# Kernel tuning notes

Hardware: AMD Instinct MI355X
Metric: run time of the kernel (lower is better)

The kernel has to match this reference:

```python
import jax, jax.numpy as jnp
import numpy as np

# Episode config: 4 episodes, 5-way 5-shot, 15 queries/class, 84x84 RGB
B, NTR, NTE, K = 4, 25, 75, 5
H = W = 84
CH = (64, 64, 128, 512)   # 4-block conv backbone channels
NUM_CLASSES = 64
SCALE_CLS = 1.0
EPS = 1e-12


def _l2norm(x, axis):
    # matches torch F.normalize(p=2, eps=1e-12)
    n = jnp.sqrt(jnp.sum(x * x, axis=axis, keepdims=True))
    return x / jnp.maximum(n, EPS)


def _conv_block(x, w, b):
    y = jax.lax.conv_general_dilated(x, w, (1, 1), 'SAME',
                                     dimension_numbers=('NCHW', 'OIHW', 'NCHW'))
    y = jax.nn.relu(y + b[None, :, None, None])
    return jax.lax.reduce_window(y, -jnp.inf, jax.lax.max,
                                 (1, 1, 2, 2), (1, 1, 2, 2), 'VALID')


def _backbone(x, ws, bs):
    for w, b in zip(ws, bs):
        x = _conv_block(x, w, b)
    return x  # (N, 512, 5, 5)


def setup_inputs() -> dict:
    key = jax.random.key(0)
    ks = jax.random.split(key, 16)
    xtrain = jax.random.normal(ks[0], (B, NTR, 3, H, W), jnp.float32)
    xtest = jax.random.normal(ks[1], (B, NTE, 3, H, W), jnp.float32)
    # one-hot support labels: 5 examples per class
    labels_tr = jnp.tile(jnp.arange(K), NTR // K)  # (NTR,)
    ytrain = jnp.tile(jax.nn.one_hot(labels_tr, K, dtype=jnp.float32)[None], (B, 1, 1))
    ytest = jax.random.randint(ks[2], (B, NTE), 0, K)
    # backbone conv params (He init)
    params = {}
    cin = 3
    for i, cout in enumerate(CH):
        scale = np.sqrt(2.0 / (cin * 9)).astype(np.float32)
        params[f'w{i+1}'] = jax.random.normal(ks[3 + i], (cout, cin, 3, 3), jnp.float32) * scale
        params[f'b{i+1}'] = jnp.zeros((cout,), jnp.float32)
        cin = cout
    params['wc'] = jax.random.normal(ks[10], (NUM_CLASSES, CH[-1]), jnp.float32) * np.sqrt(1.0 / CH[-1]).astype(np.float32)
    params['bc'] = jnp.zeros((NUM_CLASSES,), jnp.float32)
    return {'xtrain': xtrain, 'xtest': xtest, 'ytrain': ytrain, 'ytest': ytest, **params}


def reference(xtrain, xtest, ytrain, ytest,
              w1, b1, w2, b2, w3, b3, w4, b4, wc, bc):
    b, n_tr = xtrain.shape[0], xtrain.shape[1]
    n_te = xtest.shape[1]
    k = ytrain.shape[2]
    x = jnp.concatenate([xtrain.reshape(-1, 3, H, W),
                         xtest.reshape(-1, 3, H, W)], axis=0)
    f = _backbone(x, (w1, w2, w3, w4), (b1, b2, b3, b4))  # (N, c, h, w)
    c, h, w = f.shape[1], f.shape[2], f.shape[3]

    # class-averaged support prototypes (full feature maps)
    ftr = f[:b * n_tr].reshape(b, n_tr, c * h * w)
    yT = jnp.swapaxes(ytrain, 1, 2)                       # (b, k, n_tr)
    ftr = jnp.einsum('bkn,bnd->bkd', yT, ftr) / jnp.sum(yT, axis=2, keepdims=True)
    ftr = ftr.reshape(b, k, c, h, w)

    fte = f[b * n_tr:].reshape(b, n_te, c, h, w)

    # global classifier head on GAP'd, l2-normalized query features
    f_test = _l2norm(jnp.mean(fte, axis=(3, 4)).reshape(b * n_te, c), axis=1)
    predict_test = f_test @ wc.T + bc                     # (b*n_te, 64)

    # pairwise cosine scoring: original materializes (b,n2,n1,c,h,w) repeats;
    # mathematically identical einsum over the channel dim.
    ftr_avg = _l2norm(jnp.mean(ftr, axis=(3, 4)), axis=2)  # (b, k, c)
    fte_n = _l2norm(fte, axis=2)                           # (b, n_te, c, h, w)
    cls_scores = SCALE_CLS * jnp.einsum('bjchw,bic->bjihw', fte_n, ftr_avg)
    cls_scores = cls_scores.reshape(b * n_te, k, h, w)
    return predict_test, cls_scores
```

## Files before the change

kernel.cpp:

```cpp
#include <hip/hip_runtime.h>
#include <hip/hip_bf16.h>

#define DEV __device__ __forceinline__

typedef __attribute__((ext_vector_type(8))) short bf16x8;
typedef __attribute__((ext_vector_type(4))) short bf16x4;
typedef __attribute__((ext_vector_type(4))) float f32x4;

DEV unsigned short f2bf(float v) {
    union { __hip_bfloat16 b; unsigned short u; } c;
    c.b = __float2bfloat16(v);
    return c.u;
}

#define OFF_X1P   0
#define OFF_X2P   99123200
#define OFF_X3P   126208000
#define OFF_W1T   140953600
#define OFF_W2T   140964096
#define OFF_W3T   141056256
#define OFF_W4T   141240576
#define OFF_WCT   142715136
#define OFF_F4    0
#define OFF_G     20480000
#define OFF_PROTO 21299200

template<int HP, int WP, int C>
DEV void ring_zero(short* __restrict__ Xp, int img)
{
    constexpr int RING = 2 * WP + 2 * (HP - 2);
    constexpr int U = C / 8;
    short* base = Xp + (size_t)img * (HP * WP * C);
    uint4 z; z.x = z.y = z.z = z.w = 0;
    for (int i = threadIdx.x; i < RING * U; i += 256) {
        int r = i / U, u = i % U;
        int y, x;
        if (r < WP)            { y = 0;      x = r; }
        else if (r < 2 * WP)   { y = HP - 1; x = r - WP; }
        else { int s = r - 2 * WP; y = 1 + (s >> 1); x = (s & 1) ? (WP - 1) : 0; }
        *(uint4*)(base + ((size_t)(y * WP + x)) * C + u * 8) = z;
    }
}

__global__ __launch_bounds__(256)
void border_zero_all_kernel(short* __restrict__ X1p, short* __restrict__ X2p,
                            short* __restrict__ X3p)
{
    int b = blockIdx.x;
    if (b < 400)      ring_zero<44, 44, 64>(X1p, b);
    else if (b < 800) ring_zero<23, 23, 64>(X2p, b - 400);
    else              ring_zero<12, 12, 128>(X3p, b - 800);
}

template<int COUT, int CIN>
DEV void wt_tap_elem(const float* __restrict__ w, short* __restrict__ dst, int t)
{
    int cout = t / (CIN * 9), k = t % (CIN * 9);
    int tap = k / CIN, cin = k % CIN;
    float v = w[((size_t)cout * CIN + cin) * 9 + tap];
    dst[((size_t)(k >> 5) * COUT + cout) * 40 + (k & 31)] = (short)f2bf(v);
}

__global__ __launch_bounds__(256)
void wt_all_kernel(const float* __restrict__ w1, const float* __restrict__ w2,
                   const float* __restrict__ w3, const float* __restrict__ w4,
                   const float* __restrict__ wc,
                   short* __restrict__ W1t, short* __restrict__ W2t,
                   short* __restrict__ W3t, short* __restrict__ W4t,
                   float* __restrict__ wcT)
{
    int t = blockIdx.x * 256 + threadIdx.x;
    if (t < 5120) {
        int cout = t / 80, kk = t % 80;
        int tap = kk >> 2, cin = kk & 3;
        float v = (tap < 9 && cin < 3) ? w1[(cout * 3 + cin) * 9 + tap] : 0.f;
        W1t[cout * 80 + kk] = (short)f2bf(v);
        return;
    }
    t -= 5120;
    if (t < 36864) { wt_tap_elem<64, 64>(w2, W2t, t); return; }
    t -= 36864;
    if (t < 73728) { wt_tap_elem<128, 64>(w3, W3t, t); return; }
    t -= 73728;
    if (t < 589824) { wt_tap_elem<512, 128>(w4, W4t, t); return; }
    t -= 589824;
    if (t < 32768) {
        int c = t >> 6, m = t & 63;
        wcT[t] = wc[m * 512 + c];
    }
}

__global__ __launch_bounds__(256, 2)
void conv1_mfma_kernel(const float* __restrict__ xtrain, const float* __restrict__ xtest,
                       const short* __restrict__ W1t, const float* __restrict__ bias,
                       short* __restrict__ X1p)
{
    constexpr int RSTR = 352;
    __shared__ short sr[8 * RSTR];
    __shared__ float sb[64];

    const int tid = threadIdx.x;
    const int img = blockIdx.x / 14, blkrow = blockIdx.x % 14;
    const int yp0 = blkrow * 3;
    const float* src = (img < 100) ? xtrain + (size_t)img * (3 * 84 * 84)
                                   : xtest  + (size_t)(img - 100) * (3 * 84 * 84);
    const int wv = tid >> 6, lane = tid & 63, quad = lane >> 4, ln = lane & 15;

    for (int i = tid; i < 8 * 86; i += 256) {
        int r = i / 86, c = i % 86;
        int gy = 2 * yp0 - 1 + r, gx = c - 1;
        bf16x4 v = (bf16x4)0;
        if (gy >= 0 && gy < 84 && gx >= 0 && gx < 84) {
            int o = gy * 84 + gx;
            v[0] = (short)f2bf(src[o]);
            v[1] = (short)f2bf(src[7056 + o]);
            v[2] = (short)f2bf(src[14112 + o]);
        }
        *(bf16x4*)(&sr[r * RSTR + c * 4]) = v;
    }
    if (tid < 64) sb[tid] = bias[tid];

    const int t0 = 2 * quad, t1 = 2 * quad + 1;
    const int off0 = (t0 / 3) * RSTR + (t0 % 3) * 4;
    const int off1 = (t1 / 3) * RSTR + (t1 % 3) * 4;
    const int off2 = 2 * RSTR + 2 * 4;

    bf16x8 af0[4], af1[4];
    #pragma unroll
    for (int mi = 0; mi < 4; ++mi) {
        af0[mi] = *(const bf16x8*)(W1t + (mi * 16 + ln) * 80 + quad * 8);
        af1[mi] = *(const bf16x8*)(W1t + (mi * 16 + ln) * 80 + 32 + quad * 8);
    }

    f32x4 acc[4][8];
    #pragma unroll
    for (int mi = 0; mi < 4; ++mi)
        #pragma unroll
        for (int ni = 0; ni < 8; ++ni) acc[mi][ni] = (f32x4)0.f;

    __syncthreads();

    #pragma unroll
    for (int ni = 0; ni < 8; ++ni) {
        int q = wv * 128 + ni * 16 + ln;
        int qc = (q < 504) ? q : 503;
        int ypl = qc / 168, rem = qc % 168;
        int x = rem >> 1, dy = rem & 1;
        int base = (2 * ypl + dy) * RSTR + x * 4;

        bf16x4 lo0 = *(const bf16x4*)(&sr[base + off0]);
        bf16x4 hi0 = *(const bf16x4*)(&sr[base + off1]);
        bf16x8 b0;
        #pragma unroll
        for (int j = 0; j < 4; ++j) { b0[j] = lo0[j]; b0[4 + j] = hi0[j]; }
        bf16x4 lo1 = *(const bf16x4*)(&sr[base + off2]);
        bf16x8 b1;
        #pragma unroll
        for (int j = 0; j < 4; ++j) { b1[j] = lo1[j]; b1[4 + j] = lo1[j]; }

        #pragma unroll
        for (int mi = 0; mi < 4; ++mi) {
            acc[mi][ni] = __builtin_amdgcn_mfma_f32_16x16x32_bf16(b0, af0[mi], acc[mi][ni], 0, 0, 0);
            acc[mi][ni] = __builtin_amdgcn_mfma_f32_16x16x32_bf16(b1, af1[mi], acc[mi][ni], 0, 0, 0);
        }
    }

    #pragma unroll
    for (int ni = 0; ni < 8; ++ni) {
        int g = wv * 32 + ni * 4 + quad;
        bool ok = (g < 126);
        int ypl = g / 42, xg = g % 42;
        #pragma unroll
        for (int mi = 0; mi < 4; ++mi) {
            f32x4 a = acc[mi][ni];
            float m = fmaxf(fmaxf(a[0], a[1]), fmaxf(a[2], a[3]));
            if (ok) {
                int cout = mi * 16 + ln;
                unsigned short h = f2bf(fmaxf(m + sb[cout], 0.f));
                int py = yp0 + ypl;
                size_t o = (((size_t)img * 44 + py + 1) * 44 + xg + 1) * 64 + cout;
                X1p[o] = (short)h;
            }
        }
    }
}

template<int CIN, int COUT, int NWM, int NWN, int MT, int NT, int YPB,
         int WOUT, int HPIN, int WPIN, int HPO, int WPO, int RBI>
__global__ __launch_bounds__(256, 2)
void conv_mfma_kernel(const short* __restrict__ Xp, const short* __restrict__ Wt,
                      const float* __restrict__ bias, short* __restrict__ Yp)
{
    constexpr int ROWS = 2 * YPB + 2, CSTR = CIN + 8;
    constexpr int KC = CIN * 9 / 32, CPT = CIN / 32;
    constexpr int WPAIR = (2 * WOUT + 3) / 4 * 4;
    constexpr int NSLOT = YPB * WPAIR, POOLW = WOUT / 2;
    constexpr int GPR = WPAIR / 4;
    __shared__ short sx[ROWS * WPIN * CSTR];
    __shared__ float sb[COUT];

    const int tid = threadIdx.x;
    const int img = blockIdx.x / RBI, blkrow = blockIdx.x % RBI;
    const int yp0 = blkrow * YPB;
    const int wv = tid >> 6, lane = tid & 63, quad = lane >> 4, ln = lane & 15;
    const int msup = (NWM == 1) ? 0 : (wv >> 1);
    const int nsup = (NWM == 1) ? wv : (wv & 1);

    const short* xsrc = Xp + ((size_t)img * HPIN + 2 * yp0) * (WPIN * CIN);
    for (int i = tid; i < ROWS * WPIN * (CIN / 8); i += 256) {
        int g = i % (CIN / 8), pc = i / (CIN / 8);
        uint4 v = *(const uint4*)(xsrc + (size_t)pc * CIN + g * 8);
        *(uint4*)(&sx[pc * CSTR + g * 8]) = v;
    }
    for (int i = tid; i < COUT; i += 256) sb[i] = bias[i];

    int pbase[NT];
    #pragma unroll
    for (int ni = 0; ni < NT; ++ni) {
        int q = nsup * (NT * 16) + ni * 16 + ln;
        int qc = (q < NSLOT) ? q : (NSLOT - 1);
        int ypl = qc / WPAIR, rem = qc % WPAIR;
        int x = rem >> 1; if (x > WOUT - 1) x = WOUT - 1;
        int dy = rem & 1;
        pbase[ni] = (((2 * ypl + dy) * WPIN + x) * CSTR + quad * 8) * 2;
    }

    f32x4 acc[MT][NT];
    #pragma unroll
    for (int mi = 0; mi < MT; ++mi)
        #pragma unroll
        for (int ni = 0; ni < NT; ++ni) acc[mi][ni] = (f32x4)0.f;

    auto loadAF = [&](bf16x8* dst, int kc) {
        #pragma unroll
        for (int mi = 0; mi < MT; ++mi)
            dst[mi] = *(const bf16x8*)(Wt + ((size_t)kc * COUT + msup * 64 + mi * 16 + ln) * 40 + quad * 8);
    };
    auto loadBF = [&](bf16x8* dst, int kc) {
        const int tap = kc / CPT, cb = (kc % CPT) * 32;
        const int ky = tap / 3, kx = tap % 3;
        const int koff = ((ky * WPIN + kx) * CSTR + cb) * 2;
        #pragma unroll
        for (int ni = 0; ni < NT; ++ni)
            dst[ni] = *(const bf16x8*)((const char*)sx + pbase[ni] + koff);
    };

    __syncthreads();

    bf16x8 afA[MT], afB[MT], bfA[NT], bfB[NT];
    loadAF(afA, 0); loadBF(bfA, 0);
    for (int kc = 0; kc < KC; kc += 2) {
        loadAF(afB, kc + 1); loadBF(bfB, kc + 1);
        #pragma unroll
        for (int mi = 0; mi < MT; ++mi)
            #pragma unroll
            for (int ni = 0; ni < NT; ++ni)
                acc[mi][ni] = __builtin_amdgcn_mfma_f32_16x16x32_bf16(bfA[ni], afA[mi], acc[mi][ni], 0, 0, 0);
        if (kc + 2 < KC) { loadAF(afA, kc + 2); loadBF(bfA, kc + 2); }
        #pragma unroll
        for (int mi = 0; mi < MT; ++mi)
            #pragma unroll
            for (int ni = 0; ni < NT; ++ni)
                acc[mi][ni] = __builtin_amdgcn_mfma_f32_16x16x32_bf16(bfB[ni], afB[mi], acc[mi][ni], 0, 0, 0);
    }

    #pragma unroll
    for (int ni = 0; ni < NT; ++ni) {
        int g = nsup * (NT * 4) + ni * 4 + quad;
        int ypl = g / GPR, xg = g % GPR;
        bool ok = (g < NSLOT / 4) && (xg < POOLW);
        #pragma unroll
        for (int mi = 0; mi < MT; ++mi) {
            f32x4 a = acc[mi][ni];
            float m = fmaxf(fmaxf(a[0], a[1]), fmaxf(a[2], a[3]));
            if (ok) {
                int cout = msup * 64 + mi * 16 + ln;
                unsigned short h = f2bf(fmaxf(m + sb[cout], 0.f));
                int py = yp0 + ypl;
                Yp[(((size_t)img * HPO + py + 1) * WPO + xg + 1) * COUT + cout] = (short)h;
            }
        }
    }
}

__global__ __launch_bounds__(256, 2)
void conv4_mfma_kernel(const short* __restrict__ X3p, const short* __restrict__ W4t,
                       const float* __restrict__ bias, float* __restrict__ f4)
{
    constexpr int CSTR = 136;
    __shared__ short sx[144 * CSTR];
    __shared__ float sb[128];

    const int tid = threadIdx.x;
    const int img = blockIdx.x >> 2, mb = blockIdx.x & 3;
    const int wv = tid >> 6, lane = tid & 63, quad = lane >> 4, ln = lane & 15;
    const int msup = wv >> 1, nsup = wv & 1;

    const short* xsrc = X3p + (size_t)img * (144 * 128);
    for (int i = tid; i < 144 * 16; i += 256) {
        int pc = i >> 4, g = i & 15;
        uint4 v = *(const uint4*)(xsrc + pc * 128 + g * 8);
        *(uint4*)(&sx[pc * CSTR + g * 8]) = v;
    }
    for (int i = tid; i < 128; i += 256) sb[i] = bias[mb * 128 + i];

    int pbase[4];
    #pragma unroll
    for (int ni = 0; ni < 4; ++ni) {
        int q = nsup * 64 + ni * 16 + ln;
        int pc = (q < 100) ? q : 99;
        int yp = pc / 20, rem = pc % 20;
        int y = 2 * yp + (rem & 1), x = rem >> 1;
        pbase[ni] = ((y * 12 + x) * CSTR + quad * 8) * 2;
    }

    f32x4 acc[4][4];
    #pragma unroll
    for (int mi = 0; mi < 4; ++mi)
        #pragma unroll
        for (int ni = 0; ni < 4; ++ni) acc[mi][ni] = (f32x4)0.f;

    auto loadAF = [&](bf16x8* dst, int kc) {
        #pragma unroll
        for (int mi = 0; mi < 4; ++mi)
            dst[mi] = *(const bf16x8*)(W4t + ((size_t)kc * 512 + mb * 128 + msup * 64 + mi * 16 + ln) * 40 + quad * 8);
    };
    auto loadBF = [&](bf16x8* dst, int kc) {
        const int tap = kc >> 2, cb = (kc & 3) * 32;
        const int ky = tap / 3, kx = tap % 3;
        const int koff = ((ky * 12 + kx) * CSTR + cb) * 2;
        #pragma unroll
        for (int ni = 0; ni < 4; ++ni)
            dst[ni] = *(const bf16x8*)((const char*)sx + pbase[ni] + koff);
    };

    __syncthreads();

    bf16x8 afA[4], afB[4], bfA[4], bfB[4];
    loadAF(afA, 0); loadBF(bfA, 0);
    for (int kc = 0; kc < 36; kc += 2) {
        loadAF(afB, kc + 1); loadBF(bfB, kc + 1);
        #pragma unroll
        for (int mi = 0; mi < 4; ++mi)
            #pragma unroll
            for (int ni = 0; ni < 4; ++ni)
                acc[mi][ni] = __builtin_amdgcn_mfma_f32_16x16x32_bf16(bfA[ni], afA[mi], acc[mi][ni], 0, 0, 0);
        if (kc + 2 < 36) { loadAF(afA, kc + 2); loadBF(bfA, kc + 2); }
        #pragma unroll
        for (int mi = 0; mi < 4; ++mi)
            #pragma unroll
            for (int ni = 0; ni < 4; ++ni)
                acc[mi][ni] = __builtin_amdgcn_mfma_f32_16x16x32_bf16(bfB[ni], afB[mi], acc[mi][ni], 0, 0, 0);
    }

    #pragma unroll
    for (int ni = 0; ni < 4; ++ni) {
        int g = nsup * 16 + ni * 4 + quad;
        bool ok = (g < 25);
        #pragma unroll
        for (int mi = 0; mi < 4; ++mi) {
            f32x4 a = acc[mi][ni];
            float m = fmaxf(fmaxf(a[0], a[1]), fmaxf(a[2], a[3]));
            if (ok) {
                int cl = msup * 64 + mi * 16 + ln;
                f4[((size_t)img * 25 + g) * 512 + mb * 128 + cl] = fmaxf(m + sb[cl], 0.f);
            }
        }
    }
}

__global__ __launch_bounds__(256)
void gap_kernel(const float* __restrict__ f4, float* __restrict__ g)
{
    const int img = blockIdx.x;
    for (int c = threadIdx.x; c < 512; c += 256) {
        float s = 0.f;
        #pragma unroll
        for (int p = 0; p < 25; ++p)
            s += f4[((size_t)img * 25 + p) * 512 + c];
        g[(size_t)img * 512 + c] = s * (1.f / 25.f);
    }
}

__global__ __launch_bounds__(256)
void proto_kernel(const float* __restrict__ g, const float* __restrict__ ytrain,
                  float* __restrict__ proto)
{
    const int b = blockIdx.x / 5, k = blockIdx.x % 5;
    __shared__ float sp[512];
    __shared__ float red[256];

    float yv[25];
    float cnt = 0.f;
    for (int n = 0; n < 25; ++n) {
        yv[n] = ytrain[(size_t)(b * 25 + n) * 5 + k];
        cnt += yv[n];
    }
    const float icnt = 1.f / cnt;

    for (int c = threadIdx.x; c < 512; c += 256) {
        float s = 0.f;
        for (int n = 0; n < 25; ++n)
            s += yv[n] * g[((size_t)(b * 25 + n)) * 512 + c];
        sp[c] = s * icnt;
    }
    __syncthreads();

    float ss = 0.f;
    for (int c = threadIdx.x; c < 512; c += 256) ss += sp[c] * sp[c];
    red[threadIdx.x] = ss;
    __syncthreads();
    for (int s = 128; s > 0; s >>= 1) {
        if (threadIdx.x < s) red[threadIdx.x] += red[threadIdx.x + s];
        __syncthreads();
    }
    const float inv = 1.f / fmaxf(sqrtf(red[0]), 1e-12f);
    for (int c = threadIdx.x; c < 512; c += 256)
        proto[((size_t)(b * 5 + k)) * 512 + c] = sp[c] * inv;
}

__global__ __launch_bounds__(256)
void predict_kernel(const float* __restrict__ g, const float* __restrict__ wcT,
                    const float* __restrict__ bc, float* __restrict__ out)
{
    const int q = blockIdx.x;
    __shared__ float fq[512];
    __shared__ float red[256];
    __shared__ float part[4][64];

    const float* gq = g + (size_t)(100 + q) * 512;
    float ss = 0.f;
    for (int c = threadIdx.x; c < 512; c += 256) {
        const float v = gq[c];
        fq[c] = v;
        ss += v * v;
    }
    red[threadIdx.x] = ss;
    __syncthreads();
    for (int s = 128; s > 0; s >>= 1) {
        if (threadIdx.x < s) red[threadIdx.x] += red[threadIdx.x + s];
        __syncthreads();
    }
    const float inv = 1.f / fmaxf(sqrtf(red[0]), 1e-12f);

    const int cp = threadIdx.x >> 6, m = threadIdx.x & 63;
    float s = 0.f;
    const int c0 = cp * 128;
    for (int c = c0; c < c0 + 128; ++c)
        s = fmaf(fq[c], wcT[c * 64 + m], s);
    part[cp][m] = s;
    __syncthreads();
    if (threadIdx.x < 64)
        out[q * 64 + m] = (part[0][m] + part[1][m] + part[2][m] + part[3][m]) * inv + bc[m];
}

__global__ __launch_bounds__(256)
void cls_kernel(const float* __restrict__ f4, const float* __restrict__ proto,
                float* __restrict__ outc)
{
    __shared__ float sf[25 * 516];
    __shared__ float spr[5 * 516];
    __shared__ float pinv[25];
    const int q = blockIdx.x, b = q / 75;
    const float* f = f4 + (size_t)(100 + q) * (25 * 512);
    for (int i = threadIdx.x; i < 3200; i += 256) {
        int row = i >> 7, col = i & 127;
        *(float4*)(&sf[row * 516 + col * 4]) = *(const float4*)(f + row * 512 + col * 4);
    }
    const float* pb = proto + (size_t)b * 5 * 512;
    for (int i = threadIdx.x; i < 640; i += 256) {
        int row = i >> 7, col = i & 127;
        *(float4*)(&spr[row * 516 + col * 4]) = *(const float4*)(pb + row * 512 + col * 4);
    }
    __syncthreads();

    if (threadIdx.x < 25) {
        const float* fp = &sf[threadIdx.x * 516];
        float ss = 0.f;
        for (int c = 0; c < 512; c += 4) {
            float4 v = *(const float4*)(fp + c);
            ss += v.x * v.x + v.y * v.y + v.z * v.z + v.w * v.w;
        }
        pinv[threadIdx.x] = 1.f / fmaxf(sqrtf(ss), 1e-12f);
    }
    __syncthreads();

    for (int it = threadIdx.x; it < 125; it += 256) {
        int i = it / 25, p = it % 25;
        const float* fp = &sf[p * 516];
        const float* pr = &spr[i * 516];
        float dot = 0.f;
        for (int c = 0; c < 512; c += 4) {
            float4 v = *(const float4*)(fp + c);
            float4 w = *(const float4*)(pr + c);
            dot += v.x * w.x + v.y * w.y + v.z * w.z + v.w * w.w;
        }
        outc[(size_t)q * 125 + it] = dot * pinv[p];
    }
}

extern "C" void kernel_launch(void* const* d_in, const int* in_sizes, int n_in,
                              void* d_out, int out_size, void* d_ws, size_t ws_size,
                              hipStream_t stream)
{
    (void)in_sizes; (void)n_in; (void)out_size; (void)ws_size;
    const float* xtrain = (const float*)d_in[0];
    const float* xtest  = (const float*)d_in[1];
    const float* ytrain = (const float*)d_in[2];
    const float* w1 = (const float*)d_in[4];
    const float* b1 = (const float*)d_in[5];
    const float* w2 = (const float*)d_in[6];
    const float* b2 = (const float*)d_in[7];
    const float* w3 = (const float*)d_in[8];
    const float* b3 = (const float*)d_in[9];
    const float* w4 = (const float*)d_in[10];
    const float* b4 = (const float*)d_in[11];
    const float* wc = (const float*)d_in[12];
    const float* bc = (const float*)d_in[13];

    char* ws = (char*)d_ws;
    short* X1p = (short*)(ws + OFF_X1P);
    short* X2p = (short*)(ws + OFF_X2P);
    short* X3p = (short*)(ws + OFF_X3P);
    short* W1t = (short*)(ws + OFF_W1T);
    short* W2t = (short*)(ws + OFF_W2T);
    short* W3t = (short*)(ws + OFF_W3T);
    short* W4t = (short*)(ws + OFF_W4T);
    float* wcT = (float*)(ws + OFF_WCT);
    float* f4    = (float*)(ws + OFF_F4);
    float* g     = (float*)(ws + OFF_G);
    float* proto = (float*)(ws + OFF_PROTO);
    float* out = (float*)d_out;

    border_zero_all_kernel<<<1200, 256, 0, stream>>>(X1p, X2p, X3p);
    wt_all_kernel<<<2884, 256, 0, stream>>>(w1, w2, w3, w4, wc,
                                            W1t, W2t, W3t, W4t, wcT);

    conv1_mfma_kernel<<<400 * 14, 256, 0, stream>>>(xtrain, xtest, W1t, b1, X1p);
    conv_mfma_kernel< 64,  64,  1,  4, 4, 4,  3,  42,  44,  44, 23, 23,  7>
        <<<400 * 7, 256, 0, stream>>>(X1p, W2t, b2, X2p);
    conv_mfma_kernel< 64, 128,  2,  2, 4, 7,  5,  21,  23,  23, 12, 12,  2>
        <<<400 * 2, 256, 0, stream>>>(X2p, W3t, b3, X3p);
    conv4_mfma_kernel<<<400 * 4, 256, 0, stream>>>(X3p, W4t, b4, f4);

    gap_kernel<<<400, 256, 0, stream>>>(f4, g);
    proto_kernel<<<20, 256, 0, stream>>>(g, ytrain, proto);
    predict_kernel<<<300, 256, 0, stream>>>(g, wcT, bc, out);
    cls_kernel<<<300, 256, 0, stream>>>(f4, proto, out + 19200);
}
```

Before: 315.9 us.

## Fuse border zeroing into convs, GAP into conv4, merge head kernels

Removes the separate border-zeroing kernel by having each conv block zero the padding ring of its own output rows. Conv4 now handles two 128-channel slices per block (half the grid) and computes the global average pool in-kernel with shuffles and shared memory, which removes the gap kernel. The predict and cls kernels are merged into one launch. This cuts launch count and a pass over f4, but conv4 has half as many blocks, each doing twice the serial work, and adds block-wide syncs.

```diff
diff --git a/kernel.cpp b/kernel.cpp
--- a/kernel.cpp
+++ b/kernel.cpp
@@ -25,33 +25,6 @@
 #define OFF_G     20480000
 #define OFF_PROTO 21299200
 
-template<int HP, int WP, int C>
-DEV void ring_zero(short* __restrict__ Xp, int img)
-{
-    constexpr int RING = 2 * WP + 2 * (HP - 2);
-    constexpr int U = C / 8;
-    short* base = Xp + (size_t)img * (HP * WP * C);
-    uint4 z; z.x = z.y = z.z = z.w = 0;
-    for (int i = threadIdx.x; i < RING * U; i += 256) {
-        int r = i / U, u = i % U;
-        int y, x;
-        if (r < WP)            { y = 0;      x = r; }
-        else if (r < 2 * WP)   { y = HP - 1; x = r - WP; }
-        else { int s = r - 2 * WP; y = 1 + (s >> 1); x = (s & 1) ? (WP - 1) : 0; }
-        *(uint4*)(base + ((size_t)(y * WP + x)) * C + u * 8) = z;
-    }
-}
-
-__global__ __launch_bounds__(256)
-void border_zero_all_kernel(short* __restrict__ X1p, short* __restrict__ X2p,
-                            short* __restrict__ X3p)
-{
-    int b = blockIdx.x;
-    if (b < 400)      ring_zero<44, 44, 64>(X1p, b);
-    else if (b < 800) ring_zero<23, 23, 64>(X2p, b - 400);
-    else              ring_zero<12, 12, 128>(X3p, b - 800);
-}
-
 template<int COUT, int CIN>
 DEV void wt_tap_elem(const float* __restrict__ w, short* __restrict__ dst, int t)
 {
@@ -183,6 +156,26 @@
             }
         }
     }
+
+    {
+        uint4 z; z.x = z.y = z.z = z.w = 0;
+        short* yb = X1p + (size_t)img * (44 * 44 * 64);
+        for (int i = tid; i < 3 * 2 * 8; i += 256) {
+            int r = i / 16, rem = i % 16, side = rem >> 3, u = rem & 7;
+            int y = yp0 + 1 + r, x = side ? 43 : 0;
+            *(uint4*)(yb + ((size_t)(y * 44 + x)) * 64 + u * 8) = z;
+        }
+        if (blkrow == 0)
+            for (int i = tid; i < 44 * 8; i += 256) {
+                int x = i >> 3, u = i & 7;
+                *(uint4*)(yb + ((size_t)x) * 64 + u * 8) = z;
+            }
+        if (blkrow == 13)
+            for (int i = tid; i < 44 * 8; i += 256) {
+                int x = i >> 3, u = i & 7;
+                *(uint4*)(yb + ((size_t)(43 * 44 + x)) * 64 + u * 8) = z;
+            }
+    }
 }
 
 template<int CIN, int COUT, int NWM, int NWN, int MT, int NT, int YPB,
@@ -281,28 +274,51 @@
             }
         }
     }
+
+    {
+        constexpr int U = COUT / 8;
+        uint4 z; z.x = z.y = z.z = z.w = 0;
+        short* yb = Yp + (size_t)img * (HPO * WPO * COUT);
+        for (int i = tid; i < YPB * 2 * U; i += 256) {
+            int r = i / (2 * U), rem = i % (2 * U), side = rem / U, u = rem % U;
+            int y = yp0 + 1 + r, x = side ? (WPO - 1) : 0;
+            *(uint4*)(yb + ((size_t)(y * WPO + x)) * COUT + u * 8) = z;
+        }
+        if (blkrow == 0)
+            for (int i = tid; i < WPO * U; i += 256) {
+                int x = i / U, u = i % U;
+                *(uint4*)(yb + ((size_t)x) * COUT + u * 8) = z;
+            }
+        if (blkrow == RBI - 1)
+            for (int i = tid; i < WPO * U; i += 256) {
+                int x = i / U, u = i % U;
+                *(uint4*)(yb + ((size_t)((HPO - 1) * WPO + x)) * COUT + u * 8) = z;
+            }
+    }
 }
 
 __global__ __launch_bounds__(256, 2)
 void conv4_mfma_kernel(const short* __restrict__ X3p, const short* __restrict__ W4t,
-                       const float* __restrict__ bias, float* __restrict__ f4)
+                       const float* __restrict__ bias, float* __restrict__ f4,
+                       float* __restrict__ gout)
 {
     constexpr int CSTR = 136;
     __shared__ short sx[144 * CSTR];
-    __shared__ float sb[128];
+    __shared__ float sb[256];
+    __shared__ float gsum[2][128];
 
     const int tid = threadIdx.x;
-    const int img = blockIdx.x >> 2, mb = blockIdx.x & 3;
+    const int img = blockIdx.x >> 1, half = blockIdx.x & 1;
     const int wv = tid >> 6, lane = tid & 63, quad = lane >> 4, ln = lane & 15;
     const int msup = wv >> 1, nsup = wv & 1;
 
     const short* xsrc = X3p + (size_t)img * (144 * 128);
     for (int i = tid; i < 144 * 16; i += 256) {
-        int pc = i >> 4, g = i & 15;
-        uint4 v = *(const uint4*)(xsrc + pc * 128 + g * 8);
-        *(uint4*)(&sx[pc * CSTR + g * 8]) = v;
-    }
-    for (int i = tid; i < 128; i += 256) sb[i] = bias[mb * 128 + i];
+        int pc = i >> 4, u = i & 15;
+        uint4 v = *(const uint4*)(xsrc + pc * 128 + u * 8);
+        *(uint4*)(&sx[pc * CSTR + u * 8]) = v;
+    }
+    if (tid < 256) sb[tid] = bias[half * 256 + tid];
 
     int pbase[4];
     #pragma unroll
@@ -314,17 +330,6 @@
         pbase[ni] = ((y * 12 + x) * CSTR + quad * 8) * 2;
     }
 
-    f32x4 acc[4][4];
-    #pragma unroll
-    for (int mi = 0; mi < 4; ++mi)
-        #pragma unroll
-        for (int ni = 0; ni < 4; ++ni) acc[mi][ni] = (f32x4)0.f;
-
-    auto loadAF = [&](bf16x8* dst, int kc) {
-        #pragma unroll
-        for (int mi = 0; mi < 4; ++mi)
-            dst[mi] = *(const bf16x8*)(W4t + ((size_t)kc * 512 + mb * 128 + msup * 64 + mi * 16 + ln) * 40 + quad * 8);
-    };
     auto loadBF = [&](bf16x8* dst, int kc) {
         const int tap = kc >> 2, cb = (kc & 3) * 32;
         const int ky = tap / 3, kx = tap % 3;
@@ -336,49 +341,65 @@
 
     __syncthreads();
 
-    bf16x8 afA[4], afB[4], bfA[4], bfB[4];
-    loadAF(afA, 0); loadBF(bfA, 0);
-    for (int kc = 0; kc < 36; kc += 2) {
-        loadAF(afB, kc + 1); loadBF(bfB, kc + 1);
+    for (int sub = 0; sub < 2; ++sub) {
+        const int mb = half * 2 + sub;
+
+        f32x4 acc[4][4];
         #pragma unroll
         for (int mi = 0; mi < 4; ++mi)
             #pragma unroll
-            for (int ni = 0; ni < 4; ++ni)
-                acc[mi][ni] = __builtin_amdgcn_mfma_f32_16x16x32_bf16(bfA[ni], afA[mi], acc[mi][ni], 0, 0, 0);
-        if (kc + 2 < 36) { loadAF(afA, kc + 2); loadBF(bfA, kc + 2); }
-        #pragma unroll
-        for (int mi = 0; mi < 4; ++mi)
-            #pragma unroll
-            for (int ni = 0; ni < 4; ++ni)
-                acc[mi][ni] = __builtin_amdgcn_mfma_f32_16x16x32_bf16(bfB[ni], afB[mi], acc[mi][ni], 0, 0, 0);
-    }
-
-    #pragma unroll
-    for (int ni = 0; ni < 4; ++ni) {
-        int g = nsup * 16 + ni * 4 + quad;
-        bool ok = (g < 25);
+            for (int ni = 0; ni < 4; ++ni) acc[mi][ni] = (f32x4)0.f;
+
+        auto loadAF = [&](bf16x8* dst, int kc) {
+            #pragma unroll
+            for (int mi = 0; mi < 4; ++mi)
+                dst[mi] = *(const bf16x8*)(W4t + ((size_t)kc * 512 + mb * 128 + msup * 64 + mi * 16 + ln) * 40 + quad * 8);
+        };
+
+        bf16x8 afA[4], afB[4], bfA[4], bfB[4];
+        loadAF(afA, 0); loadBF(bfA, 0);
+        for (int kc = 0; kc < 36; kc += 2) {
+            loadAF(afB, kc + 1); loadBF(bfB, kc + 1);
+            #pragma unroll
+            for (int mi = 0; mi < 4; ++mi)
+                #pragma unroll
+                for (int ni = 0; ni < 4; ++ni)
+                    acc[mi][ni] = __builtin_amdgcn_mfma_f32_16x16x32_bf16(bfA[ni], afA[mi], acc[mi][ni], 0, 0, 0);
+            if (kc + 2 < 36) { loadAF(afA, kc + 2); loadBF(bfA, kc + 2); }
+            #pragma unroll
+            for (int mi = 0; mi < 4; ++mi)
+                #pragma unroll
+                for (int ni = 0; ni < 4; ++ni)
+                    acc[mi][ni] = __builtin_amdgcn_mfma_f32_16x16x32_bf16(bfB[ni], afB[mi], acc[mi][ni], 0, 0, 0);
+        }
+
+        float vsum[4] = {0.f, 0.f, 0.f, 0.f};
+        #pragma unroll
+        for (int ni = 0; ni < 4; ++ni) {
+            int gp = nsup * 16 + ni * 4 + quad;
+            bool ok = (gp < 25);
+            #pragma unroll
+            for (int mi = 0; mi < 4; ++mi) {
+                f32x4 a = acc[mi][ni];
+                float m = fmaxf(fmaxf(a[0], a[1]), fmaxf(a[2], a[3]));
+                int cl = msup * 64 + mi * 16 + ln;
+                float val = ok ? fmaxf(m + sb[sub * 128 + cl], 0.f) : 0.f;
+                if (ok) f4[((size_t)img * 25 + gp) * 512 + mb * 128 + cl] = val;
+                vsum[mi] += val;
+            }
+        }
         #pragma unroll
         for (int mi = 0; mi < 4; ++mi) {
-            f32x4 a = acc[mi][ni];
-            float m = fmaxf(fmaxf(a[0], a[1]), fmaxf(a[2], a[3]));
-            if (ok) {
-                int cl = msup * 64 + mi * 16 + ln;
-                f4[((size_t)img * 25 + g) * 512 + mb * 128 + cl] = fmaxf(m + sb[cl], 0.f);
-            }
-        }
-    }
-}
-
-__global__ __launch_bounds__(256)
-void gap_kernel(const float* __restrict__ f4, float* __restrict__ g)
-{
-    const int img = blockIdx.x;
-    for (int c = threadIdx.x; c < 512; c += 256) {
-        float s = 0.f;
-        #pragma unroll
-        for (int p = 0; p < 25; ++p)
-            s += f4[((size_t)img * 25 + p) * 512 + c];
-        g[(size_t)img * 512 + c] = s * (1.f / 25.f);
+            float v = vsum[mi];
+            v += __shfl_xor(v, 16);
+            v += __shfl_xor(v, 32);
+            if (quad == 0) gsum[nsup][msup * 64 + mi * 16 + ln] = v;
+        }
+        __syncthreads();
+        if (tid < 128)
+            gout[(size_t)img * 512 + mb * 128 + tid] =
+                (gsum[0][tid] + gsum[1][tid]) * 0.04f;
+        __syncthreads();
     }
 }
 
@@ -420,82 +441,82 @@
 }
 
 __global__ __launch_bounds__(256)
-void predict_kernel(const float* __restrict__ g, const float* __restrict__ wcT,
-                    const float* __restrict__ bc, float* __restrict__ out)
-{
-    const int q = blockIdx.x;
-    __shared__ float fq[512];
-    __shared__ float red[256];
-    __shared__ float part[4][64];
-
-    const float* gq = g + (size_t)(100 + q) * 512;
-    float ss = 0.f;
-    for (int c = threadIdx.x; c < 512; c += 256) {
-        const float v = gq[c];
-        fq[c] = v;
-        ss += v * v;
-    }
-    red[threadIdx.x] = ss;
-    __syncthreads();
-    for (int s = 128; s > 0; s >>= 1) {
-        if (threadIdx.x < s) red[threadIdx.x] += red[threadIdx.x + s];
-        __syncthreads();
-    }
-    const float inv = 1.f / fmaxf(sqrtf(red[0]), 1e-12f);
-
-    const int cp = threadIdx.x >> 6, m = threadIdx.x & 63;
-    float s = 0.f;
-    const int c0 = cp * 128;
-    for (int c = c0; c < c0 + 128; ++c)
-        s = fmaf(fq[c], wcT[c * 64 + m], s);
-    part[cp][m] = s;
-    __syncthreads();
-    if (threadIdx.x < 64)
-        out[q * 64 + m] = (part[0][m] + part[1][m] + part[2][m] + part[3][m]) * inv + bc[m];
-}
-
-__global__ __launch_bounds__(256)
-void cls_kernel(const float* __restrict__ f4, const float* __restrict__ proto,
-                float* __restrict__ outc)
-{
-    __shared__ float sf[25 * 516];
-    __shared__ float spr[5 * 516];
-    __shared__ float pinv[25];
-    const int q = blockIdx.x, b = q / 75;
-    const float* f = f4 + (size_t)(100 + q) * (25 * 512);
-    for (int i = threadIdx.x; i < 3200; i += 256) {
-        int row = i >> 7, col = i & 127;
-        *(float4*)(&sf[row * 516 + col * 4]) = *(const float4*)(f + row * 512 + col * 4);
-    }
-    const float* pb = proto + (size_t)b * 5 * 512;
-    for (int i = threadIdx.x; i < 640; i += 256) {
-        int row = i >> 7, col = i & 127;
-        *(float4*)(&spr[row * 516 + col * 4]) = *(const float4*)(pb + row * 512 + col * 4);
-    }
-    __syncthreads();
-
-    if (threadIdx.x < 25) {
-        const float* fp = &sf[threadIdx.x * 516];
+void heads_kernel(const float* __restrict__ g, const float* __restrict__ wcT,
+                  const float* __restrict__ bc, const float* __restrict__ f4,
+                  const float* __restrict__ proto, float* __restrict__ out)
+{
+    __shared__ float smem[25 * 516 + 5 * 516 + 32];
+
+    if (blockIdx.x < 300) {
+        float* fq   = smem;
+        float* red  = smem + 512;
+        float* part = smem + 768;
+        const int q = blockIdx.x;
+        const float* gq = g + (size_t)(100 + q) * 512;
         float ss = 0.f;
-        for (int c = 0; c < 512; c += 4) {
-            float4 v = *(const float4*)(fp + c);
-            ss += v.x * v.x + v.y * v.y + v.z * v.z + v.w * v.w;
-        }
-        pinv[threadIdx.x] = 1.f / fmaxf(sqrtf(ss), 1e-12f);
-    }
-    __syncthreads();
-
-    for (int it = threadIdx.x; it < 125; it += 256) {
-        int i = it / 25, p = it % 25;
-        const float* fp = &sf[p * 516];
-        const float* pr = &spr[i * 516];
-        float dot = 0.f;
-        for (int c = 0; c < 512; c += 4) {
-            float4 v = *(const float4*)(fp + c);
-            float4 w = *(const float4*)(pr + c);
-            dot += v.x * w.x + v.y * w.y + v.z * w.z + v.w * w.w;
-        }
-        outc[(size_t)q * 125 + it] = dot * pinv[p];
+        for (int c = threadIdx.x; c < 512; c += 256) {
+            const float v = gq[c];
+            fq[c] = v;
+            ss += v * v;
+        }
+        red[threadIdx.x] = ss;
+        __syncthreads();
+        for (int s = 128; s > 0; s >>= 1) {
+            if (threadIdx.x < s) red[threadIdx.x] += red[threadIdx.x + s];
+            __syncthreads();
+        }
+        const float inv = 1.f / fmaxf(sqrtf(red[0]), 1e-12f);
+
+        const int cp = threadIdx.x >> 6, m = threadIdx.x & 63;
+        float s = 0.f;
+        const int c0 = cp * 128;
+        for (int c = c0; c < c0 + 128; ++c)
+            s = fmaf(fq[c], wcT[c * 64 + m], s);
+        part[cp * 64 + m] = s;
+        __syncthreads();
+        if (threadIdx.x < 64)
+            out[q * 64 + m] = (part[m] + part[64 + m] + part[128 + m] + part[192 + m]) * inv + bc[m];
+    } else {
+        float* sf   = smem;
+        float* spr  = smem + 25 * 516;
+        float* pinv = smem + 25 * 516 + 5 * 516;
+        float* outc = out + 19200;
+        const int q = blockIdx.x - 300, b = q / 75;
+        const float* f = f4 + (size_t)(100 + q) * (25 * 512);
+        for (int i = threadIdx.x; i < 3200; i += 256) {
+            int row = i >> 7, col = i & 127;
+            *(float4*)(&sf[row * 516 + col * 4]) = *(const float4*)(f + row * 512 + col * 4);
+        }
+        const float* pb = proto + (size_t)b * 5 * 512;
+        for (int i = threadIdx.x; i < 640; i += 256) {
+            int row = i >> 7, col = i & 127;
+            *(float4*)(&spr[row * 516 + col * 4]) = *(const float4*)(pb + row * 512 + col * 4);
+        }
+        __syncthreads();
+
+        if (threadIdx.x < 25) {
+            const float* fp = &sf[threadIdx.x * 516];
+            float ss = 0.f;
+            for (int c = 0; c < 512; c += 4) {
+                float4 v = *(const float4*)(fp + c);
+                ss += v.x * v.x + v.y * v.y + v.z * v.z + v.w * v.w;
+            }
+            pinv[threadIdx.x] = 1.f / fmaxf(sqrtf(ss), 1e-12f);
+        }
+        __syncthreads();
+
+        for (int it = threadIdx.x; it < 125; it += 256) {
+            int i = it / 25, p = it % 25;
+            const float* fp = &sf[p * 516];
+            const float* pr = &spr[i * 516];
+            float dot = 0.f;
+            for (int c = 0; c < 512; c += 4) {
+                float4 v = *(const float4*)(fp + c);
+                float4 w = *(const float4*)(pr + c);
+                dot += v.x * w.x + v.y * w.y + v.z * w.z + v.w * w.w;
+            }
+            outc[(size_t)q * 125 + it] = dot * pinv[p];
+        }
     }
 }
 
@@ -532,7 +553,6 @@
     float* proto = (float*)(ws + OFF_PROTO);
     float* out = (float*)d_out;
 
-    border_zero_all_kernel<<<1200, 256, 0, stream>>>(X1p, X2p, X3p);
     wt_all_kernel<<<2884, 256, 0, stream>>>(w1, w2, w3, w4, wc,
                                             W1t, W2t, W3t, W4t, wcT);
 
@@ -541,10 +561,8 @@
         <<<400 * 7, 256, 0, stream>>>(X1p, W2t, b2, X2p);
     conv_mfma_kernel< 64, 128,  2,  2, 4, 7,  5,  21,  23,  23, 12, 12,  2>
         <<<400 * 2, 256, 0, stream>>>(X2p, W3t, b3, X3p);
-    conv4_mfma_kernel<<<400 * 4, 256, 0, stream>>>(X3p, W4t, b4, f4);
-
-    gap_kernel<<<400, 256, 0, stream>>>(f4, g);
+    conv4_mfma_kernel<<<400 * 2, 256, 0, stream>>>(X3p, W4t, b4, f4, g);
+
     proto_kernel<<<20, 256, 0, stream>>>(g, ytrain, proto);
-    predict_kernel<<<300, 256, 0, stream>>>(g, wcT, bc, out);
-    cls_kernel<<<300, 256, 0, stream>>>(f4, proto, out + 19200);
-}
+    heads_kernel<<<600, 256, 0, stream>>>(g, wcT, bc, f4, proto, out);
+}
```

New measurement: 326.2 us. +3.3%, slower.
